# Optimization experiments

Measured on AMD Instinct MI355X. Metric: run time of the kernel, lower is better.

## Reference

```python
import jax, jax.numpy as jnp
import numpy as np

B, D, C, K = 8192, 2048, 4096, 1000  # batch, input_dim, num_centers, num_classes


def setup_inputs() -> dict:
    key = jax.random.key(0)
    k0, k1, k2 = jax.random.split(key, 3)
    x = jax.random.normal(k0, (B, D), dtype=jnp.float32)
    centers = jax.random.normal(k1, (C, D), dtype=jnp.float32)
    beta = jnp.ones((C,), dtype=jnp.float32)
    W = jax.random.normal(k2, (K, C), dtype=jnp.float32) * 0.02  # fc.weight
    b = jnp.zeros((K,), dtype=jnp.float32)  # fc.bias
    return {"x": x, "centers": centers, "beta": beta, "W": W, "b": b}


def reference(x, centers, beta, W, b):
    # Pairwise Euclidean distance via the Gram trick (same math as
    # torch.norm(x[:,None,:] - centers, dim=2), without the (B,C,D) intermediate).
    x2 = jnp.sum(x * x, axis=-1, keepdims=True)          # (B, 1)
    c2 = jnp.sum(centers * centers, axis=-1)             # (C,)
    sq = x2 + c2[None, :] - 2.0 * (x @ centers.T)        # (B, C) squared distances
    dist = jnp.sqrt(jnp.maximum(sq, 0.0))
    act = jnp.exp(-beta[None, :] * dist)                 # RBF activations
    act = act / jnp.sum(act, axis=1, keepdims=True)      # normalize over centers
    return act @ W.T + b                                 # linear head (B, K)
```

## Files before the change

### kernel.cpp

```cpp
#include <hip/hip_runtime.h>


#define BB 8192
#define DD 2048
#define CC 4096
#define KK 1000
#define KP 1024

typedef unsigned short u16;
typedef __bf16 bf16x8 __attribute__((ext_vector_type(8)));
typedef float f32x16 __attribute__((ext_vector_type(16)));

typedef const void __attribute__((address_space(1)))* gvp_t;
typedef void __attribute__((address_space(3)))* lvp_t;

__device__ __forceinline__ u16 f2bf(float f) {
  union { float f; unsigned u; } v; v.f = f;
  return (u16)((v.u + 0x7fffu + ((v.u >> 16) & 1u)) >> 16);
}

__global__ void prep_norm_cast(const float* __restrict__ x, const float* __restrict__ cen,
                               u16* __restrict__ xb, u16* __restrict__ cb,
                               float* __restrict__ x2, float* __restrict__ c2) {
  int row = blockIdx.x;
  const float* src;
  u16* dst;
  float* nrm;
  if (row < BB) {
    src = x + (size_t)row * DD; dst = xb + (size_t)row * DD; nrm = x2 + row;
  } else {
    int r = row - BB;
    src = cen + (size_t)r * DD; dst = cb + (size_t)r * DD; nrm = c2 + r;
  }
  int t = threadIdx.x;
  float s = 0.f;
#pragma unroll
  for (int m = 0; m < 2; ++m) {
    int idx = t + 256 * m;
    float4 v = reinterpret_cast<const float4*>(src)[idx];
    s += v.x * v.x + v.y * v.y + v.z * v.z + v.w * v.w;
    reinterpret_cast<ushort4*>(dst)[idx] =
        make_ushort4(f2bf(v.x), f2bf(v.y), f2bf(v.z), f2bf(v.w));
  }
#pragma unroll
  for (int off = 1; off < 64; off <<= 1) s += __shfl_xor(s, off);
  __shared__ float red[4];
  if ((t & 63) == 0) red[t >> 6] = s;
  __syncthreads();
  if (t == 0) *nrm = red[0] + red[1] + red[2] + red[3];
}

__global__ void prep_wcast(const float* __restrict__ W, u16* __restrict__ wb) {
  int row = blockIdx.x;
  int t = threadIdx.x;
  ushort4* dst = reinterpret_cast<ushort4*>(wb + (size_t)row * CC);
  if (row < KK) {
    const float4* src = reinterpret_cast<const float4*>(W + (size_t)row * CC);
#pragma unroll
    for (int m = 0; m < 4; ++m) {
      float4 v = src[t + 256 * m];
      dst[t + 256 * m] = make_ushort4(f2bf(v.x), f2bf(v.y), f2bf(v.z), f2bf(v.w));
    }
  } else {
#pragma unroll
    for (int m = 0; m < 4; ++m) dst[t + 256 * m] = make_ushort4(0, 0, 0, 0);
  }
}

__global__ __launch_bounds__(256, 3)
void gemm1_rbf(const u16* __restrict__ Abf, const u16* __restrict__ Bbf,
               const float* __restrict__ x2, const float* __restrict__ c2,
               const float* __restrict__ beta, u16* __restrict__ Ebf) {
  constexpr int Kd = DD;
  __shared__ __align__(16) char smem[49152];

  const int t = threadIdx.x;
  const int lane = t & 63;
  const int wave = t >> 6;
  const int wr = wave >> 1, wc = wave & 1;
  const int l31 = lane & 31, khalf = lane >> 5;

  const int rowBase = blockIdx.y * 256;
  const int colBase = blockIdx.x * 128;

  f32x16 acc[4][2];
#pragma unroll
  for (int i = 0; i < 4; ++i)
#pragma unroll
    for (int j = 0; j < 2; ++j) acc[i][j] = 0.f;

  const int sr = t >> 3;
  const int fstage = ((t >> 3) & 7) ^ (((t >> 6) & 3) << 1);
  const int srcChunkOff = ((t & 7) ^ fstage) * 8;
  const u16* gA0 = Abf + (size_t)(rowBase + sr) * Kd + srcChunkOff;
  const u16* gB0 = Bbf + (size_t)(colBase + sr) * Kd + srcChunkOff;

  const int fv = (l31 & 7) ^ (((l31 >> 3) & 3) << 1);

  for (int kc = 0; kc < Kd; kc += 64) {
#pragma unroll
    for (int it = 0; it < 8; ++it) {
      const u16* ga = gA0 + (size_t)(32 * it) * Kd + kc;
      __builtin_amdgcn_global_load_lds((gvp_t)ga, (lvp_t)(smem + it * 4096 + t * 16), 16, 0, 0);
    }
#pragma unroll
    for (int it = 0; it < 4; ++it) {
      const u16* gb = gB0 + (size_t)(32 * it) * Kd + kc;
      __builtin_amdgcn_global_load_lds((gvp_t)gb, (lvp_t)(smem + 32768 + it * 4096 + t * 16), 16, 0, 0);
    }
    __syncthreads();
#pragma unroll
    for (int ks = 0; ks < 4; ++ks) {
      const int slot = ((ks * 2 + khalf) ^ fv) * 16;
      bf16x8 af[4], bfr[2];
#pragma unroll
      for (int i = 0; i < 4; ++i) {
        int r = wr * 128 + i * 32 + l31;
        af[i] = *(const bf16x8*)(smem + r * 128 + slot);
      }
#pragma unroll
      for (int j = 0; j < 2; ++j) {
        int r = wc * 64 + j * 32 + l31;
        bfr[j] = *(const bf16x8*)(smem + 32768 + r * 128 + slot);
      }
#pragma unroll
      for (int j = 0; j < 2; ++j)
#pragma unroll
        for (int i = 0; i < 4; ++i)
          acc[i][j] = __builtin_amdgcn_mfma_f32_32x32x16_bf16(af[i], bfr[j], acc[i][j], 0, 0, 0);
    }
    __syncthreads();
  }

  const int rbase = rowBase + wr * 128 + 4 * khalf;
  const int cbase = colBase + wc * 64;
  float c2v[2], bet[2];
  int gcol[2];
#pragma unroll
  for (int j = 0; j < 2; ++j) {
    gcol[j] = cbase + j * 32 + l31;
    c2v[j] = c2[gcol[j]];
    bet[j] = beta[gcol[j]];
  }
#pragma unroll
  for (int i = 0; i < 4; ++i) {
#pragma unroll
    for (int reg = 0; reg < 16; ++reg) {
      int grow = rbase + i * 32 + (reg & 3) + 8 * (reg >> 2);
      float x2v = x2[grow];
#pragma unroll
      for (int j = 0; j < 2; ++j) {
        float d = acc[i][j][reg];
        float sq = fmaxf(x2v + c2v[j] - 2.0f * d, 0.0f);
        float e = __expf(-bet[j] * __builtin_amdgcn_sqrtf(sq));
        Ebf[(size_t)grow * CC + gcol[j]] = f2bf(e);
      }
    }
  }
}

__global__ void rowsum_k(const u16* __restrict__ Ebf, float* __restrict__ rowsum) {
  const int lane = threadIdx.x & 63;
  const int row = blockIdx.x * 4 + (threadIdx.x >> 6);
  const uint4* p = reinterpret_cast<const uint4*>(Ebf + (size_t)row * CC);
  float s = 0.f;
#pragma unroll
  for (int it = 0; it < 8; ++it) {
    uint4 v = p[lane + 64 * it];
    unsigned w[4] = {v.x, v.y, v.z, v.w};
#pragma unroll
    for (int q = 0; q < 4; ++q) {
      union { unsigned u; float f; } lo, hi;
      lo.u = w[q] << 16;
      hi.u = w[q] & 0xffff0000u;
      s += lo.f + hi.f;
    }
  }
#pragma unroll
  for (int off = 1; off < 64; off <<= 1) s += __shfl_xor(s, off);
  if (lane == 0) rowsum[row] = s;
}

__global__ __launch_bounds__(256, 4)
void gemm2_out(const u16* __restrict__ Ebf, const u16* __restrict__ Wbf,
               float* __restrict__ out, float* __restrict__ P) {
  constexpr int Kd = CC;
  __shared__ __align__(16) char smem[32768];

  const int t = threadIdx.x;
  const int lane = t & 63;
  const int wave = t >> 6;
  const int wr = wave >> 1, wc = wave & 1;
  const int l31 = lane & 31, khalf = lane >> 5;

  const int rowBase = blockIdx.y * 128;
  const int colBase = blockIdx.x * 128;
  const int kBase = blockIdx.z * (CC / 2);

  f32x16 acc[2][2];
#pragma unroll
  for (int i = 0; i < 2; ++i)
#pragma unroll
    for (int j = 0; j < 2; ++j) acc[i][j] = 0.f;

  const int sr = t >> 3;
  const int fstage = ((t >> 3) & 7) ^ (((t >> 6) & 3) << 1);
  const int srcChunkOff = ((t & 7) ^ fstage) * 8;
  const u16* gA0 = Ebf + (size_t)(rowBase + sr) * Kd + kBase + srcChunkOff;
  const u16* gB0 = Wbf + (size_t)(colBase + sr) * Kd + kBase + srcChunkOff;
  const int fv = (l31 & 7) ^ (((l31 >> 3) & 3) << 1);

  for (int kc = 0; kc < CC / 2; kc += 64) {
#pragma unroll
    for (int it = 0; it < 4; ++it) {
      const u16* ga = gA0 + (size_t)(32 * it) * Kd + kc;
      __builtin_amdgcn_global_load_lds((gvp_t)ga, (lvp_t)(smem + it * 4096 + t * 16), 16, 0, 0);
    }
#pragma unroll
    for (int it = 0; it < 4; ++it) {
      const u16* gb = gB0 + (size_t)(32 * it) * Kd + kc;
      __builtin_amdgcn_global_load_lds((gvp_t)gb, (lvp_t)(smem + 16384 + it * 4096 + t * 16), 16, 0, 0);
    }
    __syncthreads();
#pragma unroll
    for (int ks = 0; ks < 4; ++ks) {
      const int slot = ((ks * 2 + khalf) ^ fv) * 16;
      bf16x8 af[2], bfr[2];
#pragma unroll
      for (int i = 0; i < 2; ++i) {
        int r = wr * 64 + i * 32 + l31;
        af[i] = *(const bf16x8*)(smem + r * 128 + slot);
      }
#pragma unroll
      for (int j = 0; j < 2; ++j) {
        int r = wc * 64 + j * 32 + l31;
        bfr[j] = *(const bf16x8*)(smem + 16384 + r * 128 + slot);
      }
#pragma unroll
      for (int j = 0; j < 2; ++j)
#pragma unroll
        for (int i = 0; i < 2; ++i)
          acc[i][j] = __builtin_amdgcn_mfma_f32_32x32x16_bf16(af[i], bfr[j], acc[i][j], 0, 0, 0);
    }
    __syncthreads();
  }

  const int rbase = rowBase + wr * 64 + 4 * khalf;
  const int cbase = colBase + wc * 64;
  int gcol[2];
#pragma unroll
  for (int j = 0; j < 2; ++j) gcol[j] = cbase + j * 32 + l31;

  if (blockIdx.z == 0) {
#pragma unroll
    for (int i = 0; i < 2; ++i)
#pragma unroll
      for (int reg = 0; reg < 16; ++reg) {
        int grow = rbase + i * 32 + (reg & 3) + 8 * (reg >> 2);
#pragma unroll
        for (int j = 0; j < 2; ++j)
          if (gcol[j] < KK) out[(size_t)grow * KK + gcol[j]] = acc[i][j][reg];
      }
  } else {
#pragma unroll
    for (int i = 0; i < 2; ++i)
#pragma unroll
      for (int reg = 0; reg < 16; ++reg) {
        int grow = rbase + i * 32 + (reg & 3) + 8 * (reg >> 2);
#pragma unroll
        for (int j = 0; j < 2; ++j)
          P[(size_t)grow * KP + gcol[j]] = acc[i][j][reg];
      }
  }
}

__global__ void reduce_out(float* __restrict__ out, const float* __restrict__ P,
                           const float* __restrict__ rowsum, const float* __restrict__ bias) {
  const int row = blockIdx.x;
  const int t = threadIdx.x;
  if (t < KK / 4) {
    const float inv = 1.0f / rowsum[row];
    float4 o = reinterpret_cast<const float4*>(out + (size_t)row * KK)[t];
    float4 p = reinterpret_cast<const float4*>(P + (size_t)row * KP)[t];
    float4 bv = reinterpret_cast<const float4*>(bias)[t];
    float4 r;
    r.x = (o.x + p.x) * inv + bv.x;
    r.y = (o.y + p.y) * inv + bv.y;
    r.z = (o.z + p.z) * inv + bv.z;
    r.w = (o.w + p.w) * inv + bv.w;
    reinterpret_cast<float4*>(out + (size_t)row * KK)[t] = r;
  }
}

#define OFF_XB 0u
#define OFF_CB 33554432u
#define OFF_WB 50331648u
#define OFF_EB 58720256u
#define OFF_X2 125829120u
#define OFF_C2 125861888u
#define OFF_RS 125878272u

extern "C" void kernel_launch(void* const* d_in, const int* in_sizes, int n_in,
                              void* d_out, int out_size, void* d_ws, size_t ws_size,
                              hipStream_t stream) {
  const float* x = (const float*)d_in[0];
  const float* cen = (const float*)d_in[1];
  const float* beta = (const float*)d_in[2];
  const float* W = (const float*)d_in[3];
  const float* bias = (const float*)d_in[4];
  float* out = (float*)d_out;
  char* ws = (char*)d_ws;

  u16* xb = (u16*)(ws + OFF_XB);
  u16* cb = (u16*)(ws + OFF_CB);
  u16* wb = (u16*)(ws + OFF_WB);
  u16* eb = (u16*)(ws + OFF_EB);
  float* x2 = (float*)(ws + OFF_X2);
  float* c2 = (float*)(ws + OFF_C2);
  float* rowsum = (float*)(ws + OFF_RS);
  float* P = (float*)(ws + OFF_XB);

  prep_norm_cast<<<BB + CC, 256, 0, stream>>>(x, cen, xb, cb, x2, c2);
  prep_wcast<<<KP, 256, 0, stream>>>(W, wb);
  gemm1_rbf<<<dim3(CC / 128, BB / 256), 256, 0, stream>>>(xb, cb, x2, c2, beta, eb);
  rowsum_k<<<BB / 4, 256, 0, stream>>>(eb, rowsum);
  gemm2_out<<<dim3(KP / 128, BB / 128, 2), 256, 0, stream>>>(eb, wb, out, P);
  reduce_out<<<BB, 256, 0, stream>>>(out, P, rowsum, bias);
}
```

Measured before the change: 412.3 us.

## Fold row-sum into GEMM2 via ones column in padded W and merge prep kernels

Padded row KK of the bf16 weight matrix is set to 1.0, so GEMM2 computes the per-row sum of activations in an otherwise wasted padding column. This removes the separate rowsum kernel, which re-read the whole 64MB bf16 activation matrix. The W cast is also merged into the norm/cast prep kernel to save a launch. The row sum now comes from the two K-split partials accumulated in fp32 on MFMA, which keeps the numerics close to before.

```diff
diff --git a/kernel.cpp b/kernel.cpp
--- a/kernel.cpp
+++ b/kernel.cpp
@@ -19,10 +19,29 @@
   return (u16)((v.u + 0x7fffu + ((v.u >> 16) & 1u)) >> 16);
 }
 
-__global__ void prep_norm_cast(const float* __restrict__ x, const float* __restrict__ cen,
-                               u16* __restrict__ xb, u16* __restrict__ cb,
-                               float* __restrict__ x2, float* __restrict__ c2) {
+__global__ void prep_all(const float* __restrict__ x, const float* __restrict__ cen,
+                         const float* __restrict__ W,
+                         u16* __restrict__ xb, u16* __restrict__ cb, u16* __restrict__ wb,
+                         float* __restrict__ x2, float* __restrict__ c2) {
   int row = blockIdx.x;
+  int t = threadIdx.x;
+  if (row >= BB + CC) {
+    int r = row - BB - CC;
+    ushort4* dst = reinterpret_cast<ushort4*>(wb + (size_t)r * CC);
+    if (r < KK) {
+      const float4* src = reinterpret_cast<const float4*>(W + (size_t)r * CC);
+#pragma unroll
+      for (int m = 0; m < 4; ++m) {
+        float4 v = src[t + 256 * m];
+        dst[t + 256 * m] = make_ushort4(f2bf(v.x), f2bf(v.y), f2bf(v.z), f2bf(v.w));
+      }
+    } else {
+      u16 fill = (r == KK) ? (u16)0x3F80 : (u16)0;
+#pragma unroll
+      for (int m = 0; m < 4; ++m) dst[t + 256 * m] = make_ushort4(fill, fill, fill, fill);
+    }
+    return;
+  }
   const float* src;
   u16* dst;
   float* nrm;
@@ -32,7 +51,6 @@
     int r = row - BB;
     src = cen + (size_t)r * DD; dst = cb + (size_t)r * DD; nrm = c2 + r;
   }
-  int t = threadIdx.x;
   float s = 0.f;
 #pragma unroll
   for (int m = 0; m < 2; ++m) {
@@ -50,23 +68,6 @@
   if (t == 0) *nrm = red[0] + red[1] + red[2] + red[3];
 }
 
-__global__ void prep_wcast(const float* __restrict__ W, u16* __restrict__ wb) {
-  int row = blockIdx.x;
-  int t = threadIdx.x;
-  ushort4* dst = reinterpret_cast<ushort4*>(wb + (size_t)row * CC);
-  if (row < KK) {
-    const float4* src = reinterpret_cast<const float4*>(W + (size_t)row * CC);
-#pragma unroll
-    for (int m = 0; m < 4; ++m) {
-      float4 v = src[t + 256 * m];
-      dst[t + 256 * m] = make_ushort4(f2bf(v.x), f2bf(v.y), f2bf(v.z), f2bf(v.w));
-    }
-  } else {
-#pragma unroll
-    for (int m = 0; m < 4; ++m) dst[t + 256 * m] = make_ushort4(0, 0, 0, 0);
-  }
-}
-
 __global__ __launch_bounds__(256, 3)
 void gemm1_rbf(const u16* __restrict__ Abf, const u16* __restrict__ Bbf,
                const float* __restrict__ x2, const float* __restrict__ c2,
@@ -159,31 +160,9 @@
   }
 }
 
-__global__ void rowsum_k(const u16* __restrict__ Ebf, float* __restrict__ rowsum) {
-  const int lane = threadIdx.x & 63;
-  const int row = blockIdx.x * 4 + (threadIdx.x >> 6);
-  const uint4* p = reinterpret_cast<const uint4*>(Ebf + (size_t)row * CC);
-  float s = 0.f;
-#pragma unroll
-  for (int it = 0; it < 8; ++it) {
-    uint4 v = p[lane + 64 * it];
-    unsigned w[4] = {v.x, v.y, v.z, v.w};
-#pragma unroll
-    for (int q = 0; q < 4; ++q) {
-      union { unsigned u; float f; } lo, hi;
-      lo.u = w[q] << 16;
-      hi.u = w[q] & 0xffff0000u;
-      s += lo.f + hi.f;
-    }
-  }
-#pragma unroll
-  for (int off = 1; off < 64; off <<= 1) s += __shfl_xor(s, off);
-  if (lane == 0) rowsum[row] = s;
-}
-
 __global__ __launch_bounds__(256, 4)
 void gemm2_out(const u16* __restrict__ Ebf, const u16* __restrict__ Wbf,
-               float* __restrict__ out, float* __restrict__ P) {
+               float* __restrict__ out, float* __restrict__ P, float* __restrict__ rs0) {
   constexpr int Kd = CC;
   __shared__ __align__(16) char smem[32768];
 
@@ -258,8 +237,10 @@
       for (int reg = 0; reg < 16; ++reg) {
         int grow = rbase + i * 32 + (reg & 3) + 8 * (reg >> 2);
 #pragma unroll
-        for (int j = 0; j < 2; ++j)
+        for (int j = 0; j < 2; ++j) {
           if (gcol[j] < KK) out[(size_t)grow * KK + gcol[j]] = acc[i][j][reg];
+          else if (gcol[j] == KK) rs0[grow] = acc[i][j][reg];
+        }
       }
   } else {
 #pragma unroll
@@ -275,11 +256,11 @@
 }
 
 __global__ void reduce_out(float* __restrict__ out, const float* __restrict__ P,
-                           const float* __restrict__ rowsum, const float* __restrict__ bias) {
+                           const float* __restrict__ rs0, const float* __restrict__ bias) {
   const int row = blockIdx.x;
   const int t = threadIdx.x;
   if (t < KK / 4) {
-    const float inv = 1.0f / rowsum[row];
+    const float inv = 1.0f / (rs0[row] + P[(size_t)row * KP + KK]);
     float4 o = reinterpret_cast<const float4*>(out + (size_t)row * KK)[t];
     float4 p = reinterpret_cast<const float4*>(P + (size_t)row * KP)[t];
     float4 bv = reinterpret_cast<const float4*>(bias)[t];
@@ -317,13 +298,11 @@
   u16* eb = (u16*)(ws + OFF_EB);
   float* x2 = (float*)(ws + OFF_X2);
   float* c2 = (float*)(ws + OFF_C2);
-  float* rowsum = (float*)(ws + OFF_RS);
+  float* rs0 = (float*)(ws + OFF_RS);
   float* P = (float*)(ws + OFF_XB);
 
-  prep_norm_cast<<<BB + CC, 256, 0, stream>>>(x, cen, xb, cb, x2, c2);
-  prep_wcast<<<KP, 256, 0, stream>>>(W, wb);
+  prep_all<<<BB + CC + KP, 256, 0, stream>>>(x, cen, W, xb, cb, wb, x2, c2);
   gemm1_rbf<<<dim3(CC / 128, BB / 256), 256, 0, stream>>>(xb, cb, x2, c2, beta, eb);
-  rowsum_k<<<BB / 4, 256, 0, stream>>>(eb, rowsum);
-  gemm2_out<<<dim3(KP / 128, BB / 128, 2), 256, 0, stream>>>(eb, wb, out, P);
-  reduce_out<<<BB, 256, 0, stream>>>(out, P, rowsum, bias);
-}
+  gemm2_out<<<dim3(KP / 128, BB / 128, 2), 256, 0, stream>>>(eb, wb, out, P, rs0);
+  reduce_out<<<BB, 256, 0, stream>>>(out, P, rs0, bias);
+}
```

After: 398.7 us. 3.3% less time.
